# Optimization experiments

Hardware: AMD Instinct MI355X
Metric: run time of the kernel (lower is better)

## Reference

```python
import jax, jax.numpy as jnp
import numpy as np

B, S, H = 1024, 512, 768
D1, D2 = 128, 1


def setup_inputs() -> dict:
    key = jax.random.key(0)
    k_feat, k_start, k_len, k_w1, k_w2 = jax.random.split(key, 5)
    features_extract = jax.random.normal(k_feat, (B, S, H), dtype=jnp.float32)
    start_token_idx = jax.random.randint(k_start, (B,), 1, 200, dtype=jnp.int64)
    span_len = jax.random.randint(k_len, (B,), 1, 65, dtype=jnp.int64)
    end_token_idx = start_token_idx + span_len  # guaranteed start < end <= 264 < S
    W1 = jax.random.normal(k_w1, (2 * H, D1), dtype=jnp.float32) * (1.0 / np.sqrt(2 * H))
    b1 = jnp.zeros((D1,), dtype=jnp.float32)
    W2 = jax.random.normal(k_w2, (D1, D2), dtype=jnp.float32) * (1.0 / np.sqrt(D1))
    b2 = jnp.zeros((D2,), dtype=jnp.float32)
    return {
        "features_extract": features_extract,
        "start_token_idx": start_token_idx,
        "end_token_idx": end_token_idx,
        "W1": W1, "b1": b1, "W2": W2, "b2": b2,
    }


def reference(features_extract, start_token_idx, end_token_idx, W1, b1, W2, b2):
    # CLS feature: token 0 of each example -> [B, 1, H]
    features_cls = features_extract[:, 0, :][:, None, :]

    # Ragged span mean-pool (vectorized replacement for the per-example loop):
    # mask[b, s] = start[b] <= s < end[b]
    pos = jnp.arange(features_extract.shape[1])  # [S]
    mask = (pos[None, :] >= start_token_idx[:, None]) & (pos[None, :] < end_token_idx[:, None])
    maskf = mask.astype(features_extract.dtype)  # [B, S]
    span_sum = jnp.einsum('bsh,bs->bh', features_extract, maskf)
    span_len = (end_token_idx - start_token_idx).astype(features_extract.dtype)  # >= 1
    features_crc = (span_sum / span_len[:, None])[:, None, :]  # [B, 1, H]

    # Concat + MLP head (dropout layers are identity in eval)
    features = jnp.concatenate([features_cls, features_crc], axis=2)  # [B, 1, 2H]
    h = jax.nn.relu(jnp.einsum('bid,dk->bik', features, W1) + b1)
    out = jax.nn.sigmoid(jnp.einsum('bik,ko->bio', h, W2) + b2)  # [B, 1, 1]
    return out
```

## Files before the change

### kernel.cpp

```cpp
#include <hip/hip_runtime.h>
#include <math.h>

constexpr int Bn = 1024;
constexpr int S  = 512;
constexpr int H  = 768;
constexpr int D1 = 128;
constexpr int HV = H / 4;
constexpr int K2 = 2 * H;
constexpr int NK = K2 / 32;
constexpr int NCAST = 16;

typedef _Float16 half8 __attribute__((ext_vector_type(8)));
typedef float floatx4 __attribute__((ext_vector_type(4)));


__device__ __forceinline__ size_t swz_off(int tile, int kk, int lg, int idx) {
  return ((((size_t)tile * NK + kk) * 64) + lg * 16 + idx) * 8;
}

__global__ __launch_bounds__(256) void pool_cast(
    const float* __restrict__ feat, const int* __restrict__ start,
    const int* __restrict__ endp, const float* __restrict__ W1,
    _Float16* __restrict__ gs, _Float16* __restrict__ w1s) {
  __shared__ float4 pacc[4][3][64];
  const int t = threadIdx.x;

  if (blockIdx.x < NCAST) {
    const int c  = blockIdx.x;
    const int n  = t & 127;
    const int sb = t >> 7;
    const int nt = n >> 4, ni = n & 15;
    #pragma unroll
    for (int j = 0; j < 6; ++j) {
      const int k0 = c * 96 + sb * 48 + j * 8;
      _Float16 h[8];
      #pragma unroll
      for (int i = 0; i < 8; ++i) {
        h[i] = (_Float16)W1[(size_t)(k0 + i) * D1 + n];
      }
      const int kk = k0 >> 5, lg = (k0 >> 3) & 3;
      *reinterpret_cast<half8*>(w1s + swz_off(nt, kk, lg, ni)) =
          *reinterpret_cast<half8*>(h);
    }
    return;
  }

  const int b = blockIdx.x - NCAST;
  const int eg = b >> 4, li = b & 15;
  const int w = t >> 6;
  const int l = t & 63;
  const float4* base =
      reinterpret_cast<const float4*>(feat) + (size_t)b * (S * HV);

  if (t < 192) {
    float4 cv = base[t];
    const int k = t * 4;
    const int kk = k >> 5, lg = (k >> 3) & 3, e = k & 7;
    _Float16* dst = gs + swz_off(eg, kk, lg, li) + e;
    dst[0] = (_Float16)cv.x; dst[1] = (_Float16)cv.y;
    dst[2] = (_Float16)cv.z; dst[3] = (_Float16)cv.w;
  }

  const int s0 = start[b];
  const int s1 = endp[b];

  float4 c0{0,0,0,0}, c1{0,0,0,0}, c2{0,0,0,0};
  float4 d0{0,0,0,0}, d1{0,0,0,0}, d2{0,0,0,0};
  int s = s0 + w;
  for (; s + 4 < s1; s += 8) {
    const float4* r0 = base + (size_t)s * HV;
    const float4* r1 = base + (size_t)(s + 4) * HV;
    float4 u0 = r0[l], u1 = r0[l + 64], u2 = r0[l + 128];
    float4 v0 = r1[l], v1 = r1[l + 64], v2 = r1[l + 128];
    c0.x += u0.x; c0.y += u0.y; c0.z += u0.z; c0.w += u0.w;
    c1.x += u1.x; c1.y += u1.y; c1.z += u1.z; c1.w += u1.w;
    c2.x += u2.x; c2.y += u2.y; c2.z += u2.z; c2.w += u2.w;
    d0.x += v0.x; d0.y += v0.y; d0.z += v0.z; d0.w += v0.w;
    d1.x += v1.x; d1.y += v1.y; d1.z += v1.z; d1.w += v1.w;
    d2.x += v2.x; d2.y += v2.y; d2.z += v2.z; d2.w += v2.w;
  }
  for (; s < s1; s += 4) {
    const float4* r0 = base + (size_t)s * HV;
    float4 u0 = r0[l], u1 = r0[l + 64], u2 = r0[l + 128];
    c0.x += u0.x; c0.y += u0.y; c0.z += u0.z; c0.w += u0.w;
    c1.x += u1.x; c1.y += u1.y; c1.z += u1.z; c1.w += u1.w;
    c2.x += u2.x; c2.y += u2.y; c2.z += u2.z; c2.w += u2.w;
  }
  c0.x += d0.x; c0.y += d0.y; c0.z += d0.z; c0.w += d0.w;
  c1.x += d1.x; c1.y += d1.y; c1.z += d1.z; c1.w += d1.w;
  c2.x += d2.x; c2.y += d2.y; c2.z += d2.z; c2.w += d2.w;
  pacc[w][0][l] = c0;
  pacc[w][1][l] = c1;
  pacc[w][2][l] = c2;
  __syncthreads();

  if (t < 192) {
    const int seg = t >> 6, ln = t & 63;
    float4 a = pacc[0][seg][ln], bb = pacc[1][seg][ln];
    float4 cq = pacc[2][seg][ln], dq = pacc[3][seg][ln];
    const float inv = 1.0f / (float)(s1 - s0);
    const int k = H + t * 4;
    const int kk = k >> 5, lg = (k >> 3) & 3, e = k & 7;
    _Float16* dst = gs + swz_off(eg, kk, lg, li) + e;
    dst[0] = (_Float16)(((a.x + bb.x) + (cq.x + dq.x)) * inv);
    dst[1] = (_Float16)(((a.y + bb.y) + (cq.y + dq.y)) * inv);
    dst[2] = (_Float16)(((a.z + bb.z) + (cq.z + dq.z)) * inv);
    dst[3] = (_Float16)(((a.w + bb.w) + (cq.w + dq.w)) * inv);
  }
}

__global__ __launch_bounds__(64) void head_mfma(
    const _Float16* __restrict__ gs, const _Float16* __restrict__ w1s,
    const float* __restrict__ b1, const float* __restrict__ W2,
    float* __restrict__ ts) {
  const int l  = threadIdx.x;
  const int eg = blockIdx.x & 63;
  const int nt = blockIdx.x >> 6;

  const half8* Ap = reinterpret_cast<const half8*>(gs) + (size_t)eg * NK * 64 + l;
  const half8* Bp = reinterpret_cast<const half8*>(w1s) + (size_t)nt * NK * 64 + l;

  floatx4 acc0 = {0.f, 0.f, 0.f, 0.f};
  floatx4 acc1 = {0.f, 0.f, 0.f, 0.f};
  #pragma unroll 2
  for (int kk = 0; kk < NK; kk += 4) {
    half8 a0 = Ap[(size_t)(kk + 0) * 64];
    half8 b0 = Bp[(size_t)(kk + 0) * 64];
    half8 a1 = Ap[(size_t)(kk + 1) * 64];
    half8 b1v = Bp[(size_t)(kk + 1) * 64];
    half8 a2 = Ap[(size_t)(kk + 2) * 64];
    half8 b2v = Bp[(size_t)(kk + 2) * 64];
    half8 a3 = Ap[(size_t)(kk + 3) * 64];
    half8 b3v = Bp[(size_t)(kk + 3) * 64];
    acc0 = __builtin_amdgcn_mfma_f32_16x16x32_f16(a0, b0, acc0, 0, 0, 0);
    acc1 = __builtin_amdgcn_mfma_f32_16x16x32_f16(a1, b1v, acc1, 0, 0, 0);
    acc0 = __builtin_amdgcn_mfma_f32_16x16x32_f16(a2, b2v, acc0, 0, 0, 0);
    acc1 = __builtin_amdgcn_mfma_f32_16x16x32_f16(a3, b3v, acc1, 0, 0, 0);
  }

  const int col = l & 15;
  const int n = nt * 16 + col;
  const float b1n = b1[n];
  const float w2n = W2[n];
  #pragma unroll
  for (int r = 0; r < 4; ++r) {
    float h = fmaxf((acc0[r] + acc1[r]) + b1n, 0.f) * w2n;
    h += __shfl_xor(h, 1);
    h += __shfl_xor(h, 2);
    h += __shfl_xor(h, 4);
    h += __shfl_xor(h, 8);
    if (col == 0) {
      const int m = (l >> 4) * 4 + r;
      ts[(size_t)(eg * 16 + m) * 8 + nt] = h;
    }
  }
}

__global__ __launch_bounds__(256) void fin(
    const float* __restrict__ ts, const float* __restrict__ b2,
    float* __restrict__ out) {
  const int e = blockIdx.x * 256 + threadIdx.x;
  const float4* p = reinterpret_cast<const float4*>(ts + (size_t)e * 8);
  float4 u = p[0], v = p[1];
  float s = ((u.x + u.y) + (u.z + u.w)) + ((v.x + v.y) + (v.z + v.w)) + b2[0];
  out[e] = 1.0f / (1.0f + expf(-s));
}

extern "C" void kernel_launch(void* const* d_in, const int* in_sizes, int n_in,
                              void* d_out, int out_size, void* d_ws, size_t ws_size,
                              hipStream_t stream) {
  const float* feat = (const float*)d_in[0];
  const int* start  = (const int*)d_in[1];
  const int* endp   = (const int*)d_in[2];
  const float* W1   = (const float*)d_in[3];
  const float* b1   = (const float*)d_in[4];
  const float* W2   = (const float*)d_in[5];
  const float* b2   = (const float*)d_in[6];
  float* out = (float*)d_out;

  _Float16* gs  = (_Float16*)d_ws;
  _Float16* w1s = gs + (size_t)Bn * K2;
  float* ts     = (float*)(w1s + (size_t)D1 * K2);

  hipLaunchKernelGGL(pool_cast, dim3(NCAST + Bn), dim3(256), 0, stream,
                     feat, start, endp, W1, gs, w1s);
  hipLaunchKernelGGL(head_mfma, dim3(512), dim3(64), 0, stream,
                     gs, w1s, b1, W2, ts);
  hipLaunchKernelGGL(fin, dim3(Bn / 256), dim3(256), 0, stream,
                     ts, b2, out);
}
```

Measured before the change: 33.70 us.

## Split head GEMM over K halves and move bias/ReLU/W2 reduction to final kernel

The head GEMM now splits the 1536-long K dimension into two halves across twice as many blocks (1024 instead of 512), writing raw partial sums into two fp32 planes. The final kernel adds the planes, applies b1, ReLU and the W2 dot product, reduces with wave shuffles, and applies the sigmoid. The pooled features are stored row-major with vectorized half4 writes instead of the swizzled scatter of individual halves. The aim is more parallelism in the small GEMM and cheaper pooled-feature stores. The cost is extra global traffic for the partial-sum planes (2×1024×128 floats), strided A loads in the MFMA kernel, and heavier work in the final kernel.

```diff
diff --git a/kernel.cpp b/kernel.cpp
--- a/kernel.cpp
+++ b/kernel.cpp
@@ -8,9 +8,11 @@
 constexpr int HV = H / 4;
 constexpr int K2 = 2 * H;
 constexpr int NK = K2 / 32;
+constexpr int NKH = NK / 2;
 constexpr int NCAST = 16;
 
 typedef _Float16 half8 __attribute__((ext_vector_type(8)));
+typedef _Float16 half4v __attribute__((ext_vector_type(4)));
 typedef float floatx4 __attribute__((ext_vector_type(4)));
 
 
@@ -21,7 +23,7 @@
 __global__ __launch_bounds__(256) void pool_cast(
     const float* __restrict__ feat, const int* __restrict__ start,
     const int* __restrict__ endp, const float* __restrict__ W1,
-    _Float16* __restrict__ gs, _Float16* __restrict__ w1s) {
+    _Float16* __restrict__ g16, _Float16* __restrict__ w1s) {
   __shared__ float4 pacc[4][3][64];
   const int t = threadIdx.x;
 
@@ -46,7 +48,6 @@
   }
 
   const int b = blockIdx.x - NCAST;
-  const int eg = b >> 4, li = b & 15;
   const int w = t >> 6;
   const int l = t & 63;
   const float4* base =
@@ -54,11 +55,10 @@
 
   if (t < 192) {
     float4 cv = base[t];
-    const int k = t * 4;
-    const int kk = k >> 5, lg = (k >> 3) & 3, e = k & 7;
-    _Float16* dst = gs + swz_off(eg, kk, lg, li) + e;
-    dst[0] = (_Float16)cv.x; dst[1] = (_Float16)cv.y;
-    dst[2] = (_Float16)cv.z; dst[3] = (_Float16)cv.w;
+    half4v hc;
+    hc.x = (_Float16)cv.x; hc.y = (_Float16)cv.y;
+    hc.z = (_Float16)cv.z; hc.w = (_Float16)cv.w;
+    *reinterpret_cast<half4v*>(g16 + (size_t)b * K2 + t * 4) = hc;
   }
 
   const int s0 = start[b];
@@ -99,38 +99,42 @@
     float4 a = pacc[0][seg][ln], bb = pacc[1][seg][ln];
     float4 cq = pacc[2][seg][ln], dq = pacc[3][seg][ln];
     const float inv = 1.0f / (float)(s1 - s0);
-    const int k = H + t * 4;
-    const int kk = k >> 5, lg = (k >> 3) & 3, e = k & 7;
-    _Float16* dst = gs + swz_off(eg, kk, lg, li) + e;
-    dst[0] = (_Float16)(((a.x + bb.x) + (cq.x + dq.x)) * inv);
-    dst[1] = (_Float16)(((a.y + bb.y) + (cq.y + dq.y)) * inv);
-    dst[2] = (_Float16)(((a.z + bb.z) + (cq.z + dq.z)) * inv);
-    dst[3] = (_Float16)(((a.w + bb.w) + (cq.w + dq.w)) * inv);
+    half4v r;
+    r.x = (_Float16)(((a.x + bb.x) + (cq.x + dq.x)) * inv);
+    r.y = (_Float16)(((a.y + bb.y) + (cq.y + dq.y)) * inv);
+    r.z = (_Float16)(((a.z + bb.z) + (cq.z + dq.z)) * inv);
+    r.w = (_Float16)(((a.w + bb.w) + (cq.w + dq.w)) * inv);
+    *reinterpret_cast<half4v*>(g16 + (size_t)b * K2 + H + t * 4) = r;
   }
 }
 
 __global__ __launch_bounds__(64) void head_mfma(
-    const _Float16* __restrict__ gs, const _Float16* __restrict__ w1s,
-    const float* __restrict__ b1, const float* __restrict__ W2,
-    float* __restrict__ ts) {
+    const _Float16* __restrict__ g16, const _Float16* __restrict__ w1s,
+    float* __restrict__ p0, float* __restrict__ p1) {
   const int l  = threadIdx.x;
   const int eg = blockIdx.x & 63;
-  const int nt = blockIdx.x >> 6;
+  const int rest = blockIdx.x >> 6;
+  const int nt = rest >> 1;
+  const int kh = rest & 1;
 
-  const half8* Ap = reinterpret_cast<const half8*>(gs) + (size_t)eg * NK * 64 + l;
-  const half8* Bp = reinterpret_cast<const half8*>(w1s) + (size_t)nt * NK * 64 + l;
+  const int lg = l >> 4, li = l & 15;
+  const int e0 = eg * 16;
+
+  const _Float16* Abase = g16 + (size_t)(e0 + li) * K2 + kh * (K2 / 2) + lg * 8;
+  const half8* Bp = reinterpret_cast<const half8*>(w1s) +
+                    ((size_t)nt * NK + kh * NKH) * 64 + l;
 
   floatx4 acc0 = {0.f, 0.f, 0.f, 0.f};
   floatx4 acc1 = {0.f, 0.f, 0.f, 0.f};
   #pragma unroll 2
-  for (int kk = 0; kk < NK; kk += 4) {
-    half8 a0 = Ap[(size_t)(kk + 0) * 64];
+  for (int kk = 0; kk < NKH; kk += 4) {
+    half8 a0 = *reinterpret_cast<const half8*>(Abase + (kk + 0) * 32);
     half8 b0 = Bp[(size_t)(kk + 0) * 64];
-    half8 a1 = Ap[(size_t)(kk + 1) * 64];
+    half8 a1 = *reinterpret_cast<const half8*>(Abase + (kk + 1) * 32);
     half8 b1v = Bp[(size_t)(kk + 1) * 64];
-    half8 a2 = Ap[(size_t)(kk + 2) * 64];
+    half8 a2 = *reinterpret_cast<const half8*>(Abase + (kk + 2) * 32);
     half8 b2v = Bp[(size_t)(kk + 2) * 64];
-    half8 a3 = Ap[(size_t)(kk + 3) * 64];
+    half8 a3 = *reinterpret_cast<const half8*>(Abase + (kk + 3) * 32);
     half8 b3v = Bp[(size_t)(kk + 3) * 64];
     acc0 = __builtin_amdgcn_mfma_f32_16x16x32_f16(a0, b0, acc0, 0, 0, 0);
     acc1 = __builtin_amdgcn_mfma_f32_16x16x32_f16(a1, b1v, acc1, 0, 0, 0);
@@ -138,32 +142,31 @@
     acc1 = __builtin_amdgcn_mfma_f32_16x16x32_f16(a3, b3v, acc1, 0, 0, 0);
   }
 
-  const int col = l & 15;
-  const int n = nt * 16 + col;
-  const float b1n = b1[n];
-  const float w2n = W2[n];
+  float* plane = kh ? p1 : p0;
+  const int n = nt * 16 + li;
   #pragma unroll
   for (int r = 0; r < 4; ++r) {
-    float h = fmaxf((acc0[r] + acc1[r]) + b1n, 0.f) * w2n;
-    h += __shfl_xor(h, 1);
-    h += __shfl_xor(h, 2);
-    h += __shfl_xor(h, 4);
-    h += __shfl_xor(h, 8);
-    if (col == 0) {
-      const int m = (l >> 4) * 4 + r;
-      ts[(size_t)(eg * 16 + m) * 8 + nt] = h;
-    }
+    const int m = lg * 4 + r;
+    plane[(size_t)(e0 + m) * D1 + n] = acc0[r] + acc1[r];
   }
 }
 
 __global__ __launch_bounds__(256) void fin(
-    const float* __restrict__ ts, const float* __restrict__ b2,
-    float* __restrict__ out) {
-  const int e = blockIdx.x * 256 + threadIdx.x;
-  const float4* p = reinterpret_cast<const float4*>(ts + (size_t)e * 8);
-  float4 u = p[0], v = p[1];
-  float s = ((u.x + u.y) + (u.z + u.w)) + ((v.x + v.y) + (v.z + v.w)) + b2[0];
-  out[e] = 1.0f / (1.0f + expf(-s));
+    const float* __restrict__ p0, const float* __restrict__ p1,
+    const float* __restrict__ b1, const float* __restrict__ W2,
+    const float* __restrict__ b2, float* __restrict__ out) {
+  const int t = threadIdx.x;
+  const int w = t >> 6, l = t & 63;
+  const int e = blockIdx.x * 4 + w;
+  const int k0 = l, k1 = l + 64;
+  const size_t base = (size_t)e * D1;
+  float h0 = b1[k0] + p0[base + k0] + p1[base + k0];
+  float h1 = b1[k1] + p0[base + k1] + p1[base + k1];
+  h0 = fmaxf(h0, 0.f); h1 = fmaxf(h1, 0.f);
+  float v = h0 * W2[k0] + h1 * W2[k1];
+  #pragma unroll
+  for (int off = 32; off > 0; off >>= 1) v += __shfl_down(v, off);
+  if (l == 0) out[e] = 1.0f / (1.0f + expf(-(v + b2[0])));
 }
 
 extern "C" void kernel_launch(void* const* d_in, const int* in_sizes, int n_in,
@@ -178,14 +181,15 @@
   const float* b2   = (const float*)d_in[6];
   float* out = (float*)d_out;
 
-  _Float16* gs  = (_Float16*)d_ws;
-  _Float16* w1s = gs + (size_t)Bn * K2;
-  float* ts     = (float*)(w1s + (size_t)D1 * K2);
+  _Float16* g16 = (_Float16*)d_ws;
+  _Float16* w1s = g16 + (size_t)Bn * K2;
+  float* p0     = (float*)(w1s + (size_t)D1 * K2);
+  float* p1     = p0 + (size_t)Bn * D1;
 
   hipLaunchKernelGGL(pool_cast, dim3(NCAST + Bn), dim3(256), 0, stream,
-                     feat, start, endp, W1, gs, w1s);
-  hipLaunchKernelGGL(head_mfma, dim3(512), dim3(64), 0, stream,
-                     gs, w1s, b1, W2, ts);
-  hipLaunchKernelGGL(fin, dim3(Bn / 256), dim3(256), 0, stream,
-                     ts, b2, out);
+                     feat, start, endp, W1, g16, w1s);
+  hipLaunchKernelGGL(head_mfma, dim3(1024), dim3(64), 0, stream,
+                     g16, w1s, p0, p1);
+  hipLaunchKernelGGL(fin, dim3(Bn / 4), dim3(256), 0, stream,
+                     p0, p1, b1, W2, b2, out);
 }
```

New measurement: 31.94 us. -5.2%, faster.
